# Performance work log

Hardware: AMD Instinct MI355X
Metric: run time of the kernel (lower is better)

Reference implementation:

```python
import jax, jax.numpy as jnp
import numpy as np

NUM_CLASSES = 20
MEM_SIZE = 512      # memory_bank_size
MAX_VIEWS = 512
TEMP = 0.1
MOMENTUM = 0.999
IGNORE_IDX = 255
AUX_IDX = 254
EPS = 1e-12


def _nearest_resize(gt, Ho, Wo):
    # torch F.interpolate(mode='nearest'): src = floor(dst * in/out)
    B, Hi, Wi = gt.shape
    ri = (jnp.arange(Ho) * Hi) // Ho
    ci = (jnp.arange(Wo) * Wi) // Wo
    return gt[:, ri][:, :, ci]


def _norm_flat(p):
    # L2-normalize over channels, then [B, C, H, W] -> [B, H*W, C]
    p = p / jnp.maximum(jnp.linalg.norm(p, axis=1, keepdims=True), EPS)
    B, C = p.shape[0], p.shape[1]
    return p.reshape(B, C, -1).transpose(0, 2, 1)


def setup_inputs() -> dict:
    key = jax.random.key(0)
    k1, k2, k3, k4, k5 = jax.random.split(key, 5)
    B, D, H, W = 4, 256, 128, 128
    Hg, Wg = 512, 512
    return {
        'main_proj': jax.random.normal(k1, (B, D, H, W), dtype=jnp.float32),
        'main_gt': jax.random.randint(k2, (B, Hg, Wg), 0, NUM_CLASSES).astype(jnp.int64),
        'aux_proj': jax.random.normal(k3, (B, D, H, W), dtype=jnp.float32),
        'aux_gt': jax.random.randint(k4, (B, Hg, Wg), 0, NUM_CLASSES).astype(jnp.int64),
        'memory_bank': jax.random.normal(k5, (NUM_CLASSES, MEM_SIZE, D), dtype=jnp.float32),
    }


def reference(main_proj, main_gt, aux_proj, aux_gt, memory_bank):
    C, M, D = memory_bank.shape
    B, _, H, W = main_proj.shape
    mg = _nearest_resize(main_gt, H, W)
    ag = _nearest_resize(aux_gt, aux_proj.shape[2], aux_proj.shape[3])

    embd = jnp.concatenate([_norm_flat(main_proj), _norm_flat(aux_proj)], axis=1)
    embd = embd.reshape(-1, D)                       # [N, D]
    label = jnp.concatenate([mg.reshape(B, -1), ag.reshape(B, -1)], axis=1).reshape(-1)

    valid = label != IGNORE_IDX
    label = jnp.where(label == AUX_IDX, C - 1, label)

    # per-class gather: stable argsort puts class-c pixels first (deterministic
    # stand-in for torch.randperm selection)
    masks = (label[None, :] == jnp.arange(C)[:, None]) & valid[None, :]   # [C, N]
    counts = masks.sum(axis=1)                                           # [C]
    order = jnp.argsort(~masks, axis=1, stable=True)[:, :M]              # [C, M]
    sel = embd[order]                                                    # [C, M, D]
    sel_valid = jnp.arange(M)[None, :] < counts[:, None]                 # [C, M]

    # momentum scatter-update to memory bank (no grad through features)
    upd = MOMENTUM * memory_bank + (1.0 - MOMENTUM) * jax.lax.stop_gradient(sel)
    upd = upd / jnp.maximum(jnp.linalg.norm(upd, axis=2, keepdims=True), EPS)
    bank = jnp.where(sel_valid[..., None], upd, memory_bank)             # [C, M, D]

    # anchors from current batch (with grad)
    V = min(MAX_VIEWS, M)
    anchors = sel[:, :V].reshape(C * V, D)
    a_valid = sel_valid[:, :V].reshape(-1)
    a_lbl = jnp.repeat(jnp.arange(C), V)

    # contrastive samples from updated bank (constant w.r.t. grad)
    contras = bank.reshape(C * M, D)
    c_valid = jnp.linalg.norm(bank, axis=2).reshape(-1) > 0
    c_lbl = jnp.repeat(jnp.arange(C), M)

    # InfoNCE with masked softmax over valid contrastive columns
    scores = (anchors @ contras.T) / TEMP                                # [A, K]
    scores = jnp.where(c_valid[None, :], scores, -1e9)
    logp = jax.nn.log_softmax(scores, axis=1)
    pos = ((a_lbl[:, None] == c_lbl[None, :]) & c_valid[None, :]).astype(scores.dtype)
    pos_sum = (pos * logp).sum(axis=1)
    pos_cnt = pos.sum(axis=1)
    va = (pos_cnt > 0) & a_valid
    mlpp = jnp.where(va, pos_sum / jnp.maximum(pos_cnt, 1.0), 0.0)
    loss = -mlpp.sum() / jnp.maximum(va.sum(), 1).astype(scores.dtype)
    return loss
```

## Files before the change

### kernel.cpp

```cpp
#include <hip/hip_runtime.h>
#include <cstdint>
#include <math.h>

#define NCLS  20
#define MSZ   512
#define DIM   256
#define HW    16384
#define NPIX  131072
#define AROWS 10240
#define TEMP_INV 10.0f
#define EXP2K 14.4269504088896f

typedef __attribute__((ext_vector_type(8))) short bf16x8;
typedef __attribute__((ext_vector_type(4))) float f32x4;

__device__ __forceinline__ short f2bf(float f) {
    unsigned u = __float_as_uint(f);
    unsigned r = (u + 0x7FFFu + ((u >> 16) & 1u)) >> 16;
    return (short)r;
}
__device__ __forceinline__ float bf2f(short s) {
    return __uint_as_float(((unsigned)(unsigned short)s) << 16);
}
__device__ __forceinline__ float fexp2(float x) {
    float r;
    asm volatile("v_exp_f32 %0, %1" : "=v"(r) : "v"(x));
    return r;
}

__device__ __forceinline__ void gld16(const void* g, void* l) {
    __builtin_amdgcn_global_load_lds(
        (const __attribute__((address_space(1))) unsigned int*)(uintptr_t)g,
        (__attribute__((address_space(3))) unsigned int*)(unsigned int)(uintptr_t)l,
        16, 0, 0);
}

__global__ __launch_bounds__(256) void k_hist(const int* __restrict__ mg,
                                              const int* __restrict__ ag,
                                              int* __restrict__ labels,
                                              int* __restrict__ hist,
                                              int* __restrict__ counts,
                                              int* __restrict__ pix2row) {
    int chunk = blockIdx.x, t = threadIdx.x;
    int lane = t & 63;
    int n = chunk * 256 + t;
    int b = n >> 15, r = n & 32767;
    const int* g = (r < HW) ? mg : ag;
    int p = (r < HW) ? r : (r - HW);
    int h = p >> 7, w = p & 127;
    int lab = g[(((size_t)b * 512) + (size_t)(h << 2)) * 512 + (size_t)(w << 2)];
    if (lab == 255) lab = -1;
    else if (lab == 254) lab = NCLS - 1;
    labels[n] = lab;
    pix2row[n] = -1;

    __shared__ int cnt20[NCLS];
    if (t < NCLS) cnt20[t] = 0;
    __syncthreads();
#pragma unroll
    for (int c = 0; c < NCLS; ++c) {
        unsigned long long m = __ballot(lab == c);
        if (lane == 0 && m) atomicAdd(&cnt20[c], __popcll(m));
    }
    __syncthreads();
    if (t < NCLS) {
        hist[t * 512 + chunk] = cnt20[t];
        atomicAdd(&counts[t], cnt20[t]);
    }
}

__global__ __launch_bounds__(256) void k_write(const int* __restrict__ labels,
                                               const int* __restrict__ hist,
                                               int* __restrict__ pix2row) {
    int chunk = blockIdx.x, t = threadIdx.x;
    int lane = t & 63, wv = t >> 6;
    __shared__ int cbase[NCLS];
    __shared__ int wcnt2[4][NCLS];

#pragma unroll
    for (int cc = 0; cc < 5; ++cc) {
        int c = wv * 5 + cc;
        int s = 0;
        for (int j = lane; j < chunk; j += 64) s += hist[c * 512 + j];
#pragma unroll
        for (int o = 32; o > 0; o >>= 1) s += __shfl_down(s, o, 64);
        if (lane == 0) cbase[c] = s;
    }

    int n = chunk * 256 + t;
    int lab = labels[n];
    int myrank = 0;
#pragma unroll
    for (int c = 0; c < NCLS; ++c) {
        unsigned long long m = __ballot(lab == c);
        if (lane == 0) wcnt2[wv][c] = __popcll(m);
        if (lab == c) myrank = __popcll(m & ((1ull << lane) - 1ull));
    }
    __syncthreads();
    if (lab >= 0) {
        int base = cbase[lab] + myrank;
        for (int w = 0; w < wv; ++w) base += wcnt2[w][lab];
        if (base < MSZ) pix2row[n] = lab * MSZ + base;
    }
}

__global__ __launch_bounds__(256) void k_scatter(const float* __restrict__ mainp,
                                                 const float* __restrict__ auxp,
                                                 const int* __restrict__ pix2row,
                                                 float* __restrict__ xF) {
    int idx = blockIdx.x * 256 + threadIdx.x;
    int p4 = idx & 4095;
    int ch = (idx >> 12) & 255;
    int bs = idx >> 20;
    int b = bs >> 1, src = bs & 1;
    const float* base = (src ? auxp : mainp) + (size_t)b * DIM * HW + (size_t)ch * HW;
    float4 v = *(const float4*)(base + p4 * 4);
    int4 pr = *(const int4*)(pix2row + bs * HW + p4 * 4);
    if (pr.x >= 0) xF[(size_t)pr.x * DIM + ch] = v.x;
    if (pr.y >= 0) xF[(size_t)pr.y * DIM + ch] = v.y;
    if (pr.z >= 0) xF[(size_t)pr.z * DIM + ch] = v.z;
    if (pr.w >= 0) xF[(size_t)pr.w * DIM + ch] = v.w;
}

__global__ __launch_bounds__(256) void k_normbank(const float* __restrict__ xF,
                                                  const float* __restrict__ bank,
                                                  const int* __restrict__ counts,
                                                  short* __restrict__ anchorsB,
                                                  short* __restrict__ contrasB,
                                                  int* __restrict__ c_valid) {
    int lane = threadIdx.x & 63, wv = threadIdx.x >> 6;
    int a = blockIdx.x * 4 + wv;
    float4 xv = *(const float4*)&xF[(size_t)a * DIM + lane * 4];
    float x[4] = {xv.x, xv.y, xv.z, xv.w};
    float ss = x[0]*x[0] + x[1]*x[1] + x[2]*x[2] + x[3]*x[3];
#pragma unroll
    for (int o = 1; o < 64; o <<= 1) ss += __shfl_xor(ss, o, 64);
    float scale = 1.0f / fmaxf(sqrtf(ss), 1e-12f);
    float ax[4];
#pragma unroll
    for (int q = 0; q < 4; ++q) ax[q] = x[q] * scale;
    short4 oa;
    oa.x = f2bf(ax[0]); oa.y = f2bf(ax[1]); oa.z = f2bf(ax[2]); oa.w = f2bf(ax[3]);
    *(short4*)&anchorsB[(size_t)a * DIM + lane * 4] = oa;

    int cc = a >> 9, m2 = a & 511;
    bool upd = m2 < counts[cc];
    float4 bv = *(const float4*)&bank[(size_t)a * DIM + lane * 4];
    float u[4];
    u[0] = upd ? 0.999f * bv.x + 0.001f * ax[0] : bv.x;
    u[1] = upd ? 0.999f * bv.y + 0.001f * ax[1] : bv.y;
    u[2] = upd ? 0.999f * bv.z + 0.001f * ax[2] : bv.z;
    u[3] = upd ? 0.999f * bv.w + 0.001f * ax[3] : bv.w;
    float ss2 = u[0]*u[0] + u[1]*u[1] + u[2]*u[2] + u[3]*u[3];
#pragma unroll
    for (int o = 1; o < 64; o <<= 1) ss2 += __shfl_xor(ss2, o, 64);
    float nrm = sqrtf(ss2);
    float inv = 1.0f / fmaxf(nrm, 1e-12f);
    short4 oc;
    oc.x = f2bf(upd ? u[0] * inv : bv.x);
    oc.y = f2bf(upd ? u[1] * inv : bv.y);
    oc.z = f2bf(upd ? u[2] * inv : bv.z);
    oc.w = f2bf(upd ? u[3] * inv : bv.w);
    *(short4*)&contrasB[(size_t)a * DIM + lane * 4] = oc;
    if (lane == 0) c_valid[a] = (nrm > 0.0f) ? 1 : 0;
}

__global__ __launch_bounds__(256) void k_csum(const short* __restrict__ contrasB,
                                              const int* __restrict__ c_valid,
                                              float* __restrict__ S,
                                              int* __restrict__ pcnt) {
    int c = blockIdx.x >> 3, oct = blockIdx.x & 7;
    int t = threadIdx.x;
    int rs = t >> 5, cs = t & 31;
    int row0 = c * MSZ + oct * 64;
    float acc[8] = {0,0,0,0,0,0,0,0};
    int cnt = 0;
#pragma unroll
    for (int m8 = 0; m8 < 8; ++m8) {
        int row = row0 + m8 * 8 + rs;
        int v = c_valid[row];
        bf16x8 x = *(const bf16x8*)&contrasB[(size_t)row * DIM + cs * 8];
        if (v) {
#pragma unroll
            for (int j = 0; j < 8; ++j) acc[j] += bf2f(x[j]);
        }
        if (cs == 0) cnt += v;
    }
    __shared__ float sacc[8][DIM];
    __shared__ int scnt[8];
#pragma unroll
    for (int j = 0; j < 8; ++j) sacc[rs][cs * 8 + j] = acc[j];
    if (cs == 0) scnt[rs] = cnt;
    __syncthreads();
    float s = 0.0f;
#pragma unroll
    for (int r = 0; r < 8; ++r) s += sacc[r][t];
    atomicAdd(&S[c * DIM + t], s);
    if (t == 0) {
        int tot = 0;
#pragma unroll
        for (int r = 0; r < 8; ++r) tot += scnt[r];
        atomicAdd(&pcnt[c], tot);
    }
}

#define TSM 256
#define TSN 256
__global__ __launch_bounds__(512, 2) void k_score(const short* __restrict__ A,
                                                  const short* __restrict__ Bc,
                                                  const int* __restrict__ c_valid,
                                                  float* __restrict__ row_sumexp) {
    __shared__ short As[2][TSM * 32];
    __shared__ short Bs[2][TSN * 32];
    int t = threadIdx.x;
    int lane = t & 63, wv = t >> 6;
    int wr = wv & 3, wc = wv >> 2;
    int row0 = blockIdx.x * TSM, col0 = blockIdx.y * TSN;
    int lrow = lane >> 2;
    int gseg = (lane & 3) ^ (lrow & 3);
    int qr = lane >> 4, qc = lane & 15;

    f32x4 acc[4][8] = {};

    const short* Ag = A  + (size_t)row0 * DIM;
    const short* Bg = Bc + (size_t)col0 * DIM;

    auto stage = [&](int buf, int k0) {
#pragma unroll
        for (int g = 0; g < 4; ++g) {
            int f = wv * 4 + g;
            if (f < 16) {
                gld16(Ag + (size_t)(f * 16 + lrow) * DIM + k0 + gseg * 8,
                      &As[buf][(f * 16) * 32]);
            } else {
                gld16(Bg + (size_t)((f - 16) * 16 + lrow) * DIM + k0 + gseg * 8,
                      &Bs[buf][((f - 16) * 16) * 32]);
            }
        }
    };

    stage(0, 0);
#pragma unroll
    for (int k = 0; k < 8; ++k) {
        int cur = k & 1;
        if (k < 7) {
            stage(cur ^ 1, (k + 1) * 32);
            asm volatile("s_waitcnt vmcnt(4)" ::: "memory");
        } else {
            asm volatile("s_waitcnt vmcnt(0)" ::: "memory");
        }
        asm volatile("s_barrier" ::: "memory");

        bf16x8 af[4], bfv[8];
        int slot = (qr ^ (qc & 3)) * 8;
#pragma unroll
        for (int i = 0; i < 4; ++i)
            af[i] = *(const bf16x8*)&As[cur][(wr * 64 + i * 16 + qc) * 32 + slot];
#pragma unroll
        for (int j = 0; j < 8; ++j)
            bfv[j] = *(const bf16x8*)&Bs[cur][(wc * 128 + j * 16 + qc) * 32 + slot];
#pragma unroll
        for (int i = 0; i < 4; ++i)
#pragma unroll
            for (int j = 0; j < 8; ++j)
                acc[i][j] = __builtin_amdgcn_mfma_f32_16x16x32_bf16(af[i], bfv[j], acc[i][j], 0, 0, 0);

        if (k < 7) asm volatile("s_barrier" ::: "memory");
    }

    float cm[8];
#pragma unroll
    for (int j = 0; j < 8; ++j)
        cm[j] = c_valid[col0 + wc * 128 + j * 16 + qc] ? 1.0f : 0.0f;
#pragma unroll
    for (int i = 0; i < 4; ++i)
#pragma unroll
        for (int r = 0; r < 4; ++r) {
            float e = 0.0f;
#pragma unroll
            for (int j = 0; j < 8; ++j)
                e += cm[j] * fexp2(acc[i][j][r] * EXP2K);
#pragma unroll
            for (int o = 1; o < 16; o <<= 1) e += __shfl_xor(e, o, 64);
            if (qc == 0)
                atomicAdd(&row_sumexp[row0 + wr * 64 + i * 16 + qr * 4 + r], e);
        }
}

__global__ __launch_bounds__(256) void k_fin1(const short* __restrict__ anchorsB,
                                              const float* __restrict__ S,
                                              const int* __restrict__ counts,
                                              const int* __restrict__ pcnt,
                                              const float* __restrict__ row_sumexp,
                                              float* __restrict__ rowterm,
                                              int* __restrict__ rowvld) {
    int lane = threadIdx.x & 63, wv = threadIdx.x >> 6;
    int a = blockIdx.x * 4 + wv;
    int c = a >> 9, m = a & 511;
    short4 a4 = *(const short4*)&anchorsB[(size_t)a * DIM + lane * 4];
    float4 s4 = *(const float4*)&S[c * DIM + lane * 4];
    float dot = bf2f(a4.x) * s4.x + bf2f(a4.y) * s4.y + bf2f(a4.z) * s4.z + bf2f(a4.w) * s4.w;
#pragma unroll
    for (int o = 1; o < 64; o <<= 1) dot += __shfl_xor(dot, o, 64);
    if (lane == 0) {
        int pc = pcnt[c];
        bool va = (m < counts[c]) && (pc > 0);
        float v = 0.0f;
        if (va) {
            float lse = logf(row_sumexp[a]);
            v = (TEMP_INV * dot - (float)pc * lse) / (float)pc;
        }
        rowterm[a] = v;
        rowvld[a] = va ? 1 : 0;
    }
}

__global__ __launch_bounds__(256) void k_fin2(const float* __restrict__ rowterm,
                                              const int* __restrict__ rowvld,
                                              float* __restrict__ out) {
    __shared__ float sred[4];
    __shared__ int cred[4];
    int t = threadIdx.x;
    float lsum = 0.0f;
    int vcnt = 0;
    for (int a = t; a < AROWS; a += 256) {
        lsum += rowterm[a];
        vcnt += rowvld[a];
    }
#pragma unroll
    for (int o = 32; o > 0; o >>= 1) {
        lsum += __shfl_down(lsum, o, 64);
        vcnt += __shfl_down(vcnt, o, 64);
    }
    if ((t & 63) == 0) { sred[t >> 6] = lsum; cred[t >> 6] = vcnt; }
    __syncthreads();
    if (t == 0) {
        float L = sred[0] + sred[1] + sred[2] + sred[3];
        int V = cred[0] + cred[1] + cred[2] + cred[3];
        out[0] = -L / (float)(V > 0 ? V : 1);
    }
}

extern "C" void kernel_launch(void* const* d_in, const int* in_sizes, int n_in,
                              void* d_out, int out_size, void* d_ws, size_t ws_size,
                              hipStream_t stream) {
    const float* main_proj = (const float*)d_in[0];
    const int*   main_gt   = (const int*)d_in[1];
    const float* aux_proj  = (const float*)d_in[2];
    const int*   aux_gt    = (const int*)d_in[3];
    const float* bank      = (const float*)d_in[4];
    float* out = (float*)d_out;

    char* ws = (char*)d_ws;
    int*   labels     = (int*)ws;
    float* rowterm    = (float*)ws;
    int*   rowvld     = (int*)(ws + 40960);
    int*   hist       = (int*)(ws + 524288);
    int*   pix2row    = (int*)(ws + 565248);
    int*   c_valid    = (int*)(ws + 1089536);
    float* row_sumexp = (float*)(ws + 1130496);
    float* S          = (float*)(ws + 1171456);
    int*   pcnt       = (int*)(ws + 1191936);
    int*   counts     = (int*)(ws + 1192192);
    float* xF         = (float*)(ws + 1192448);
    short* anchorsB   = (short*)(ws + 11678208);
    short* contrasB   = (short*)(ws + 16921088);

    hipMemsetAsync(ws + 1130496, 0, 61952, stream);
    k_hist<<<512, 256, 0, stream>>>(main_gt, aux_gt, labels, hist, counts, pix2row);
    k_write<<<512, 256, 0, stream>>>(labels, hist, pix2row);
    k_scatter<<<32768, 256, 0, stream>>>(main_proj, aux_proj, pix2row, xF);
    k_normbank<<<AROWS / 4, 256, 0, stream>>>(xF, bank, counts,
                                              anchorsB, contrasB, c_valid);
    k_csum<<<NCLS * 8, 256, 0, stream>>>(contrasB, c_valid, S, pcnt);
    dim3 grid(AROWS / TSM, AROWS / TSN);
    k_score<<<grid, 512, 0, stream>>>(anchorsB, contrasB, c_valid, row_sumexp);
    k_fin1<<<AROWS / 4, 256, 0, stream>>>(anchorsB, S, counts, pcnt, row_sumexp,
                                          rowterm, rowvld);
    k_fin2<<<1, 256, 0, stream>>>(rowterm, rowvld, out);
}
```

Measured before the change: 298.4 us.

## Fuse pipeline kernels, drop memset, and retile score GEMM to 128x256

Zeroing of the accumulation region moves into k_hist, which removes the memset. Class counts are now derived inside k_write instead of through atomics. Normalization, bank update and class sums are fused into one kernel, and the two finalize kernels merge into one using a last-block-done atomic pattern. The score GEMM tile shrinks from 256x256 to 128x256 with higher occupancy bounds, trading data reuse for more blocks and fewer launches overall.

```diff
diff --git a/kernel.cpp b/kernel.cpp
--- a/kernel.cpp
+++ b/kernel.cpp
@@ -27,7 +27,6 @@
     asm volatile("v_exp_f32 %0, %1" : "=v"(r) : "v"(x));
     return r;
 }
-
 __device__ __forceinline__ void gld16(const void* g, void* l) {
     __builtin_amdgcn_global_load_lds(
         (const __attribute__((address_space(1))) unsigned int*)(uintptr_t)g,
@@ -35,15 +34,20 @@
         16, 0, 0);
 }
 
+#define ZREG_FLOATS 15488
+
 __global__ __launch_bounds__(256) void k_hist(const int* __restrict__ mg,
                                               const int* __restrict__ ag,
                                               int* __restrict__ labels,
                                               int* __restrict__ hist,
-                                              int* __restrict__ counts,
-                                              int* __restrict__ pix2row) {
+                                              int* __restrict__ pix2row,
+                                              float* __restrict__ zreg) {
     int chunk = blockIdx.x, t = threadIdx.x;
     int lane = t & 63;
-    int n = chunk * 256 + t;
+    int gi = chunk * 256 + t;
+    if (gi < ZREG_FLOATS) zreg[gi] = 0.0f;
+
+    int n = gi;
     int b = n >> 15, r = n & 32767;
     const int* g = (r < HW) ? mg : ag;
     int p = (r < HW) ? r : (r - HW);
@@ -63,15 +67,13 @@
         if (lane == 0 && m) atomicAdd(&cnt20[c], __popcll(m));
     }
     __syncthreads();
-    if (t < NCLS) {
-        hist[t * 512 + chunk] = cnt20[t];
-        atomicAdd(&counts[t], cnt20[t]);
-    }
+    if (t < NCLS) hist[t * 512 + chunk] = cnt20[t];
 }
 
 __global__ __launch_bounds__(256) void k_write(const int* __restrict__ labels,
                                                const int* __restrict__ hist,
-                                               int* __restrict__ pix2row) {
+                                               int* __restrict__ pix2row,
+                                               int* __restrict__ counts) {
     int chunk = blockIdx.x, t = threadIdx.x;
     int lane = t & 63, wv = t >> 6;
     __shared__ int cbase[NCLS];
@@ -102,6 +104,8 @@
         for (int w = 0; w < wv; ++w) base += wcnt2[w][lab];
         if (base < MSZ) pix2row[n] = lab * MSZ + base;
     }
+    if (chunk == 511 && t < NCLS)
+        counts[t] = cbase[t] + wcnt2[0][t] + wcnt2[1][t] + wcnt2[2][t] + wcnt2[3][t];
 }
 
 __global__ __launch_bounds__(256) void k_scatter(const float* __restrict__ mainp,
@@ -122,121 +126,104 @@
     if (pr.w >= 0) xF[(size_t)pr.w * DIM + ch] = v.w;
 }
 
-__global__ __launch_bounds__(256) void k_normbank(const float* __restrict__ xF,
-                                                  const float* __restrict__ bank,
-                                                  const int* __restrict__ counts,
-                                                  short* __restrict__ anchorsB,
-                                                  short* __restrict__ contrasB,
-                                                  int* __restrict__ c_valid) {
-    int lane = threadIdx.x & 63, wv = threadIdx.x >> 6;
-    int a = blockIdx.x * 4 + wv;
-    float4 xv = *(const float4*)&xF[(size_t)a * DIM + lane * 4];
-    float x[4] = {xv.x, xv.y, xv.z, xv.w};
-    float ss = x[0]*x[0] + x[1]*x[1] + x[2]*x[2] + x[3]*x[3];
-#pragma unroll
-    for (int o = 1; o < 64; o <<= 1) ss += __shfl_xor(ss, o, 64);
-    float scale = 1.0f / fmaxf(sqrtf(ss), 1e-12f);
-    float ax[4];
-#pragma unroll
-    for (int q = 0; q < 4; ++q) ax[q] = x[q] * scale;
-    short4 oa;
-    oa.x = f2bf(ax[0]); oa.y = f2bf(ax[1]); oa.z = f2bf(ax[2]); oa.w = f2bf(ax[3]);
-    *(short4*)&anchorsB[(size_t)a * DIM + lane * 4] = oa;
-
-    int cc = a >> 9, m2 = a & 511;
-    bool upd = m2 < counts[cc];
-    float4 bv = *(const float4*)&bank[(size_t)a * DIM + lane * 4];
-    float u[4];
-    u[0] = upd ? 0.999f * bv.x + 0.001f * ax[0] : bv.x;
-    u[1] = upd ? 0.999f * bv.y + 0.001f * ax[1] : bv.y;
-    u[2] = upd ? 0.999f * bv.z + 0.001f * ax[2] : bv.z;
-    u[3] = upd ? 0.999f * bv.w + 0.001f * ax[3] : bv.w;
-    float ss2 = u[0]*u[0] + u[1]*u[1] + u[2]*u[2] + u[3]*u[3];
-#pragma unroll
-    for (int o = 1; o < 64; o <<= 1) ss2 += __shfl_xor(ss2, o, 64);
-    float nrm = sqrtf(ss2);
-    float inv = 1.0f / fmaxf(nrm, 1e-12f);
-    short4 oc;
-    oc.x = f2bf(upd ? u[0] * inv : bv.x);
-    oc.y = f2bf(upd ? u[1] * inv : bv.y);
-    oc.z = f2bf(upd ? u[2] * inv : bv.z);
-    oc.w = f2bf(upd ? u[3] * inv : bv.w);
-    *(short4*)&contrasB[(size_t)a * DIM + lane * 4] = oc;
-    if (lane == 0) c_valid[a] = (nrm > 0.0f) ? 1 : 0;
-}
-
-__global__ __launch_bounds__(256) void k_csum(const short* __restrict__ contrasB,
-                                              const int* __restrict__ c_valid,
-                                              float* __restrict__ S,
-                                              int* __restrict__ pcnt) {
-    int c = blockIdx.x >> 3, oct = blockIdx.x & 7;
-    int t = threadIdx.x;
-    int rs = t >> 5, cs = t & 31;
-    int row0 = c * MSZ + oct * 64;
-    float acc[8] = {0,0,0,0,0,0,0,0};
-    int cnt = 0;
-#pragma unroll
-    for (int m8 = 0; m8 < 8; ++m8) {
-        int row = row0 + m8 * 8 + rs;
-        int v = c_valid[row];
-        bf16x8 x = *(const bf16x8*)&contrasB[(size_t)row * DIM + cs * 8];
-        if (v) {
-#pragma unroll
-            for (int j = 0; j < 8; ++j) acc[j] += bf2f(x[j]);
-        }
-        if (cs == 0) cnt += v;
-    }
-    __shared__ float sacc[8][DIM];
-    __shared__ int scnt[8];
-#pragma unroll
-    for (int j = 0; j < 8; ++j) sacc[rs][cs * 8 + j] = acc[j];
-    if (cs == 0) scnt[rs] = cnt;
-    __syncthreads();
-    float s = 0.0f;
-#pragma unroll
-    for (int r = 0; r < 8; ++r) s += sacc[r][t];
+__global__ __launch_bounds__(256) void k_nbc(const float* __restrict__ xF,
+                                             const float* __restrict__ bank,
+                                             const int* __restrict__ counts,
+                                             short* __restrict__ anchorsB,
+                                             short* __restrict__ contrasB,
+                                             int* __restrict__ c_valid,
+                                             float* __restrict__ S,
+                                             int* __restrict__ pcnt) {
+    int blk = blockIdx.x;
+    int c = blk >> 3;
+    int t = threadIdx.x, lane = t & 63, wv = t >> 6;
+    int cc = counts[c];
+    int base = blk * 64;
+    float sacc[4] = {0.f, 0.f, 0.f, 0.f};
+    int vcnt = 0;
+
+    for (int it = 0; it < 16; ++it) {
+        int a = base + it * 4 + wv;
+        int m = a & 511;
+        float4 xv = *(const float4*)&xF[(size_t)a * DIM + lane * 4];
+        float x[4] = {xv.x, xv.y, xv.z, xv.w};
+        float ss = x[0]*x[0] + x[1]*x[1] + x[2]*x[2] + x[3]*x[3];
+#pragma unroll
+        for (int o = 1; o < 64; o <<= 1) ss += __shfl_xor(ss, o, 64);
+        float scale = 1.0f / fmaxf(sqrtf(ss), 1e-12f);
+        float ax[4];
+#pragma unroll
+        for (int q = 0; q < 4; ++q) ax[q] = x[q] * scale;
+        short4 oa;
+        oa.x = f2bf(ax[0]); oa.y = f2bf(ax[1]); oa.z = f2bf(ax[2]); oa.w = f2bf(ax[3]);
+        *(short4*)&anchorsB[(size_t)a * DIM + lane * 4] = oa;
+
+        bool upd = m < cc;
+        float4 bv = *(const float4*)&bank[(size_t)a * DIM + lane * 4];
+        float u[4];
+        u[0] = upd ? 0.999f * bv.x + 0.001f * ax[0] : bv.x;
+        u[1] = upd ? 0.999f * bv.y + 0.001f * ax[1] : bv.y;
+        u[2] = upd ? 0.999f * bv.z + 0.001f * ax[2] : bv.z;
+        u[3] = upd ? 0.999f * bv.w + 0.001f * ax[3] : bv.w;
+        float ss2 = u[0]*u[0] + u[1]*u[1] + u[2]*u[2] + u[3]*u[3];
+#pragma unroll
+        for (int o = 1; o < 64; o <<= 1) ss2 += __shfl_xor(ss2, o, 64);
+        float nrm = sqrtf(ss2);
+        float inv = 1.0f / fmaxf(nrm, 1e-12f);
+        short oc[4];
+        oc[0] = f2bf(upd ? u[0] * inv : bv.x);
+        oc[1] = f2bf(upd ? u[1] * inv : bv.y);
+        oc[2] = f2bf(upd ? u[2] * inv : bv.z);
+        oc[3] = f2bf(upd ? u[3] * inv : bv.w);
+        *(short4*)&contrasB[(size_t)a * DIM + lane * 4] = *(short4*)oc;
+        bool valid = nrm > 0.0f;
+        if (lane == 0) {
+            c_valid[a] = valid ? 1 : 0;
+            vcnt += valid ? 1 : 0;
+        }
+        if (valid) {
+#pragma unroll
+            for (int q = 0; q < 4; ++q) sacc[q] += bf2f(oc[q]);
+        }
+    }
+
+    __shared__ float s4[4][DIM];
+    __shared__ int pv[4];
+#pragma unroll
+    for (int q = 0; q < 4; ++q) s4[wv][lane * 4 + q] = sacc[q];
+    if (lane == 0) pv[wv] = vcnt;
+    __syncthreads();
+    float s = s4[0][t] + s4[1][t] + s4[2][t] + s4[3][t];
     atomicAdd(&S[c * DIM + t], s);
-    if (t == 0) {
-        int tot = 0;
-#pragma unroll
-        for (int r = 0; r < 8; ++r) tot += scnt[r];
-        atomicAdd(&pcnt[c], tot);
-    }
-}
-
-#define TSM 256
-#define TSN 256
-__global__ __launch_bounds__(512, 2) void k_score(const short* __restrict__ A,
+    if (t == 0) atomicAdd(&pcnt[c], pv[0] + pv[1] + pv[2] + pv[3]);
+}
+
+__global__ __launch_bounds__(512, 4) void k_score(const short* __restrict__ A,
                                                   const short* __restrict__ Bc,
                                                   const int* __restrict__ c_valid,
                                                   float* __restrict__ row_sumexp) {
-    __shared__ short As[2][TSM * 32];
-    __shared__ short Bs[2][TSN * 32];
+    __shared__ short As[2][128 * 32];
+    __shared__ short Bs[2][256 * 32];
     int t = threadIdx.x;
     int lane = t & 63, wv = t >> 6;
-    int wr = wv & 3, wc = wv >> 2;
-    int row0 = blockIdx.x * TSM, col0 = blockIdx.y * TSN;
+    int wr = wv & 1, wc = wv >> 1;
+    int row0 = blockIdx.x * 128, col0 = blockIdx.y * 256;
     int lrow = lane >> 2;
     int gseg = (lane & 3) ^ (lrow & 3);
     int qr = lane >> 4, qc = lane & 15;
 
-    f32x4 acc[4][8] = {};
+    f32x4 acc[4][4] = {};
 
     const short* Ag = A  + (size_t)row0 * DIM;
     const short* Bg = Bc + (size_t)col0 * DIM;
 
     auto stage = [&](int buf, int k0) {
-#pragma unroll
-        for (int g = 0; g < 4; ++g) {
-            int f = wv * 4 + g;
-            if (f < 16) {
-                gld16(Ag + (size_t)(f * 16 + lrow) * DIM + k0 + gseg * 8,
-                      &As[buf][(f * 16) * 32]);
-            } else {
-                gld16(Bg + (size_t)((f - 16) * 16 + lrow) * DIM + k0 + gseg * 8,
-                      &Bs[buf][((f - 16) * 16) * 32]);
-            }
-        }
+        gld16(Ag + (size_t)(wv * 16 + lrow) * DIM + k0 + gseg * 8,
+              &As[buf][(wv * 16) * 32]);
+        gld16(Bg + (size_t)(wv * 32 + lrow) * DIM + k0 + gseg * 8,
+              &Bs[buf][(wv * 32) * 32]);
+        gld16(Bg + (size_t)(wv * 32 + 16 + lrow) * DIM + k0 + gseg * 8,
+              &Bs[buf][(wv * 32 + 16) * 32]);
     };
 
     stage(0, 0);
@@ -245,41 +232,41 @@
         int cur = k & 1;
         if (k < 7) {
             stage(cur ^ 1, (k + 1) * 32);
-            asm volatile("s_waitcnt vmcnt(4)" ::: "memory");
+            asm volatile("s_waitcnt vmcnt(3)" ::: "memory");
         } else {
             asm volatile("s_waitcnt vmcnt(0)" ::: "memory");
         }
         asm volatile("s_barrier" ::: "memory");
 
-        bf16x8 af[4], bfv[8];
+        bf16x8 af[4], bfv[4];
         int slot = (qr ^ (qc & 3)) * 8;
 #pragma unroll
         for (int i = 0; i < 4; ++i)
             af[i] = *(const bf16x8*)&As[cur][(wr * 64 + i * 16 + qc) * 32 + slot];
 #pragma unroll
-        for (int j = 0; j < 8; ++j)
-            bfv[j] = *(const bf16x8*)&Bs[cur][(wc * 128 + j * 16 + qc) * 32 + slot];
+        for (int j = 0; j < 4; ++j)
+            bfv[j] = *(const bf16x8*)&Bs[cur][(wc * 64 + j * 16 + qc) * 32 + slot];
 #pragma unroll
         for (int i = 0; i < 4; ++i)
 #pragma unroll
-            for (int j = 0; j < 8; ++j)
+            for (int j = 0; j < 4; ++j)
                 acc[i][j] = __builtin_amdgcn_mfma_f32_16x16x32_bf16(af[i], bfv[j], acc[i][j], 0, 0, 0);
 
         if (k < 7) asm volatile("s_barrier" ::: "memory");
     }
 
-    float cm[8];
-#pragma unroll
-    for (int j = 0; j < 8; ++j)
-        cm[j] = c_valid[col0 + wc * 128 + j * 16 + qc] ? 1.0f : 0.0f;
+    float cm[4];
+#pragma unroll
+    for (int j = 0; j < 4; ++j)
+        cm[j] = c_valid[col0 + wc * 64 + j * 16 + qc] ? 1.0f : 0.0f;
 #pragma unroll
     for (int i = 0; i < 4; ++i)
 #pragma unroll
         for (int r = 0; r < 4; ++r) {
-            float e = 0.0f;
-#pragma unroll
-            for (int j = 0; j < 8; ++j)
-                e += cm[j] * fexp2(acc[i][j][r] * EXP2K);
+            float e = cm[0] * fexp2(acc[i][0][r] * EXP2K)
+                    + cm[1] * fexp2(acc[i][1][r] * EXP2K)
+                    + cm[2] * fexp2(acc[i][2][r] * EXP2K)
+                    + cm[3] * fexp2(acc[i][3][r] * EXP2K);
 #pragma unroll
             for (int o = 1; o < 16; o <<= 1) e += __shfl_xor(e, o, 64);
             if (qc == 0)
@@ -287,57 +274,49 @@
         }
 }
 
-__global__ __launch_bounds__(256) void k_fin1(const short* __restrict__ anchorsB,
-                                              const float* __restrict__ S,
-                                              const int* __restrict__ counts,
-                                              const int* __restrict__ pcnt,
-                                              const float* __restrict__ row_sumexp,
-                                              float* __restrict__ rowterm,
-                                              int* __restrict__ rowvld) {
-    int lane = threadIdx.x & 63, wv = threadIdx.x >> 6;
-    int a = blockIdx.x * 4 + wv;
-    int c = a >> 9, m = a & 511;
-    short4 a4 = *(const short4*)&anchorsB[(size_t)a * DIM + lane * 4];
-    float4 s4 = *(const float4*)&S[c * DIM + lane * 4];
-    float dot = bf2f(a4.x) * s4.x + bf2f(a4.y) * s4.y + bf2f(a4.z) * s4.z + bf2f(a4.w) * s4.w;
-#pragma unroll
-    for (int o = 1; o < 64; o <<= 1) dot += __shfl_xor(dot, o, 64);
-    if (lane == 0) {
-        int pc = pcnt[c];
-        bool va = (m < counts[c]) && (pc > 0);
-        float v = 0.0f;
-        if (va) {
+__global__ __launch_bounds__(256) void k_fin(const short* __restrict__ anchorsB,
+                                             const float* __restrict__ S,
+                                             const int* __restrict__ counts,
+                                             const int* __restrict__ pcnt,
+                                             const float* __restrict__ row_sumexp,
+                                             float* __restrict__ facc,
+                                             int* __restrict__ done_cnt,
+                                             float* __restrict__ out) {
+    int blk = blockIdx.x;
+    int c = blk >> 3;
+    int t = threadIdx.x, lane = t & 63, wv = t >> 6;
+    int pc = pcnt[c], cc = counts[c];
+    float lsum = 0.0f, vc = 0.0f;
+
+    for (int it = 0; it < 16; ++it) {
+        int a = blk * 64 + it * 4 + wv;
+        short4 a4 = *(const short4*)&anchorsB[(size_t)a * DIM + lane * 4];
+        float4 s4 = *(const float4*)&S[c * DIM + lane * 4];
+        float dot = bf2f(a4.x) * s4.x + bf2f(a4.y) * s4.y
+                  + bf2f(a4.z) * s4.z + bf2f(a4.w) * s4.w;
+#pragma unroll
+        for (int o = 1; o < 64; o <<= 1) dot += __shfl_xor(dot, o, 64);
+        if (lane == 0 && (a & 511) < cc && pc > 0) {
             float lse = logf(row_sumexp[a]);
-            v = (TEMP_INV * dot - (float)pc * lse) / (float)pc;
-        }
-        rowterm[a] = v;
-        rowvld[a] = va ? 1 : 0;
-    }
-}
-
-__global__ __launch_bounds__(256) void k_fin2(const float* __restrict__ rowterm,
-                                              const int* __restrict__ rowvld,
-                                              float* __restrict__ out) {
-    __shared__ float sred[4];
-    __shared__ int cred[4];
-    int t = threadIdx.x;
-    float lsum = 0.0f;
-    int vcnt = 0;
-    for (int a = t; a < AROWS; a += 256) {
-        lsum += rowterm[a];
-        vcnt += rowvld[a];
-    }
-#pragma unroll
-    for (int o = 32; o > 0; o >>= 1) {
-        lsum += __shfl_down(lsum, o, 64);
-        vcnt += __shfl_down(vcnt, o, 64);
-    }
-    if ((t & 63) == 0) { sred[t >> 6] = lsum; cred[t >> 6] = vcnt; }
+            lsum += (TEMP_INV * dot - (float)pc * lse) / (float)pc;
+            vc += 1.0f;
+        }
+    }
+
+    __shared__ float wls[4], wvc[4];
+    if (lane == 0) { wls[wv] = lsum; wvc[wv] = vc; }
     __syncthreads();
     if (t == 0) {
-        float L = sred[0] + sred[1] + sred[2] + sred[3];
-        int V = cred[0] + cred[1] + cred[2] + cred[3];
-        out[0] = -L / (float)(V > 0 ? V : 1);
+        atomicAdd(&facc[0], wls[0] + wls[1] + wls[2] + wls[3]);
+        atomicAdd(&facc[1], wvc[0] + wvc[1] + wvc[2] + wvc[3]);
+        __threadfence();
+        unsigned d = atomicAdd((unsigned*)done_cnt, 1u);
+        if (d == 159u) {
+            __threadfence();
+            float L = atomicAdd(&facc[0], 0.0f);
+            float V = atomicAdd(&facc[1], 0.0f);
+            out[0] = -L / fmaxf(V, 1.0f);
+        }
     }
 }
 
@@ -353,29 +332,27 @@
 
     char* ws = (char*)d_ws;
     int*   labels     = (int*)ws;
-    float* rowterm    = (float*)ws;
-    int*   rowvld     = (int*)(ws + 40960);
     int*   hist       = (int*)(ws + 524288);
     int*   pix2row    = (int*)(ws + 565248);
     int*   c_valid    = (int*)(ws + 1089536);
-    float* row_sumexp = (float*)(ws + 1130496);
-    float* S          = (float*)(ws + 1171456);
-    int*   pcnt       = (int*)(ws + 1191936);
-    int*   counts     = (int*)(ws + 1192192);
-    float* xF         = (float*)(ws + 1192448);
-    short* anchorsB   = (short*)(ws + 11678208);
-    short* contrasB   = (short*)(ws + 16921088);
-
-    hipMemsetAsync(ws + 1130496, 0, 61952, stream);
-    k_hist<<<512, 256, 0, stream>>>(main_gt, aux_gt, labels, hist, counts, pix2row);
-    k_write<<<512, 256, 0, stream>>>(labels, hist, pix2row);
+    float* zreg       = (float*)(ws + 1130496);
+    float* row_sumexp = zreg;
+    float* S          = zreg + 10240;
+    int*   pcnt       = (int*)(zreg + 15360);
+    float* facc       = zreg + 15380;
+    int*   done_cnt   = (int*)(zreg + 15382);
+    int*   counts     = (int*)(ws + 1192448);
+    float* xF         = (float*)(ws + 1192704);
+    short* anchorsB   = (short*)(ws + 11678464);
+    short* contrasB   = (short*)(ws + 16921344);
+
+    k_hist<<<512, 256, 0, stream>>>(main_gt, aux_gt, labels, hist, pix2row, zreg);
+    k_write<<<512, 256, 0, stream>>>(labels, hist, pix2row, counts);
     k_scatter<<<32768, 256, 0, stream>>>(main_proj, aux_proj, pix2row, xF);
-    k_normbank<<<AROWS / 4, 256, 0, stream>>>(xF, bank, counts,
-                                              anchorsB, contrasB, c_valid);
-    k_csum<<<NCLS * 8, 256, 0, stream>>>(contrasB, c_valid, S, pcnt);
-    dim3 grid(AROWS / TSM, AROWS / TSN);
+    k_nbc<<<AROWS / 64, 256, 0, stream>>>(xF, bank, counts, anchorsB, contrasB,
+                                          c_valid, S, pcnt);
+    dim3 grid(AROWS / 128, AROWS / 256);
     k_score<<<grid, 512, 0, stream>>>(anchorsB, contrasB, c_valid, row_sumexp);
-    k_fin1<<<AROWS / 4, 256, 0, stream>>>(anchorsB, S, counts, pcnt, row_sumexp,
-                                          rowterm, rowvld);
-    k_fin2<<<1, 256, 0, stream>>>(rowterm, rowvld, out);
-}
+    k_fin<<<AROWS / 64, 256, 0, stream>>>(anchorsB, S, counts, pcnt, row_sumexp,
+                                          facc, done_cnt, out);
+}
```

New measurement: 297.1 us. Within noise of the previous version (-0.5%).
